# Optimization experiments

Measured on AMD Instinct MI355X. Metric: run time of the kernel, lower is better.

The kernel has to match this reference:

```python
import math
import jax, jax.numpy as jnp
import numpy as np

EMBED_DIM = 1024
NUM_HEADS = 16
HEAD_DIM = EMBED_DIM // NUM_HEADS


def _xavier(key, fan_in, fan_out):
    lim = math.sqrt(6.0 / (fan_in + fan_out))
    return jax.random.uniform(key, (fan_out, fan_in), jnp.float32, -lim, lim)


def setup_inputs() -> dict:
    key = jax.random.key(0)
    kx, kq, kk, kv, ko = jax.random.split(key, 5)
    B, L = 4, 2048
    x = jax.random.normal(kx, (B, L, EMBED_DIM), jnp.float32)
    return {
        "x": x,
        "wq": _xavier(kq, EMBED_DIM, EMBED_DIM), "bq": jnp.zeros((EMBED_DIM,), jnp.float32),
        "wk": _xavier(kk, EMBED_DIM, EMBED_DIM), "bk": jnp.zeros((EMBED_DIM,), jnp.float32),
        "wv": _xavier(kv, EMBED_DIM, EMBED_DIM), "bv": jnp.zeros((EMBED_DIM,), jnp.float32),
        "wo": _xavier(ko, EMBED_DIM, EMBED_DIM), "bo": jnp.zeros((EMBED_DIM,), jnp.float32),
    }


def reference(x, wq, bq, wk, bk, wv, bv, wo, bo):
    B, L, D = x.shape
    H, Dh = NUM_HEADS, HEAD_DIM

    def proj(w, b):
        # nn.Linear: x @ w.T + b, then split heads -> (B, H, L, Dh)
        return (jnp.einsum('bld,ed->ble', x, w) + b).reshape(B, L, H, Dh).transpose(0, 2, 1, 3)

    q, k, v = proj(wq, bq), proj(wk, bk), proj(wv, bv)
    # NOTE: original torch code scales by sqrt(key.size(dim=1)) == sqrt(num_heads)
    scale = 1.0 / math.sqrt(H)
    scores = jnp.einsum('bhqd,bhkd->bhqk', q, k) * scale  # (B, H, L, L)
    attn = jax.nn.softmax(scores, axis=-1)
    out = jnp.einsum('bhqk,bhkd->bhqd', attn, v)          # (B, H, L, Dh)
    out = out.transpose(0, 2, 1, 3).reshape(B, L, D)
    return jnp.einsum('bld,ed->ble', out, wo) + bo
```

## Files before the change

### kernel.cpp

```cpp
#include <hip/hip_runtime.h>
#include <hip/hip_bf16.h>

#define DEVI __device__ __forceinline__

using u16 = unsigned short;
typedef __attribute__((ext_vector_type(8))) short bf16x8;
typedef __attribute__((ext_vector_type(4))) short bf16x4;
typedef __attribute__((ext_vector_type(4))) float f32x4;

constexpr int Bb = 4, Ls = 2048, Dd = 1024, Hh = 16, DhC = 64;
constexpr int Mm = Bb * Ls;

DEVI u16 f2bf(float f) {
  union { float f; unsigned u; } x; x.f = f;
  unsigned r = x.u + 0x7FFFu + ((x.u >> 16) & 1u);
  return (u16)(r >> 16);
}
DEVI float bf2f(u16 b) {
  union { unsigned u; float f; } x; x.u = ((unsigned)b) << 16;
  return x.f;
}

DEVI unsigned cvt_pk_bf16(float a, float b) {
  unsigned d;
  asm("v_cvt_pk_bf16_f32 %0, %1, %2" : "=v"(d) : "v"(a), "v"(b));
  return d;
}

DEVI void gload_lds16(const u16* g, u16* l) {
  __builtin_amdgcn_global_load_lds(
      (const __attribute__((address_space(1))) unsigned int*)g,
      (__attribute__((address_space(3))) unsigned int*)l, 16, 0, 0);
}

DEVI bf16x8 ld_frag(const u16* p) { return *reinterpret_cast<const bf16x8*>(p); }

__global__ void cvt_all(const float* __restrict__ x,
                        const float* __restrict__ wq, const float* __restrict__ wk,
                        const float* __restrict__ wv, const float* __restrict__ wo,
                        u16* __restrict__ xb,
                        u16* __restrict__ wqb, u16* __restrict__ wkb,
                        u16* __restrict__ wvb, u16* __restrict__ wob) {
  const int tid = blockIdx.x * blockDim.x + threadIdx.x;
  constexpr int NT = 2048 * 256;
  constexpr int N4X = Mm * Dd / 4;
  constexpr int N4W = Dd * Dd / 4;
  for (int i = tid; i < N4X; i += NT) {
    float4 v = reinterpret_cast<const float4*>(x)[i];
    reinterpret_cast<ushort4*>(xb)[i] =
        make_ushort4(f2bf(v.x), f2bf(v.y), f2bf(v.z), f2bf(v.w));
  }
  for (int i = tid; i < 4 * N4W; i += NT) {
    int which = i / N4W, off = i - which * N4W;
    const float* s = which == 0 ? wq : which == 1 ? wk : which == 2 ? wv : wo;
    u16* d = which == 0 ? wqb : which == 1 ? wkb : which == 2 ? wvb : wob;
    float4 v = reinterpret_cast<const float4*>(s)[off];
    reinterpret_cast<ushort4*>(d)[off] =
        make_ushort4(f2bf(v.x), f2bf(v.y), f2bf(v.z), f2bf(v.w));
  }
}

__global__ __launch_bounds__(512) void gemm_qkv256(
    const u16* __restrict__ A, const u16* __restrict__ W,
    const float* __restrict__ bq, const float* __restrict__ bk2,
    const float* __restrict__ bv,
    u16* __restrict__ qm, u16* __restrict__ km, u16* __restrict__ vt)
{
  constexpr int K = 1024, BK = 64, NSTEP = K / BK;
  __shared__ u16 lds[2][2][256 * 64];

  const int tid = threadIdx.x;
  const int wave = tid >> 6, lane = tid & 63;
  const int wr = wave >> 2, wc = wave & 3;
  const int lrow = lane & 15, hi = lane >> 4, lk = hi * 8;
  const int swz = (lrow & 7) << 3;
  const int m0 = blockIdx.y * 256;
  const int n0g = blockIdx.x * 256;

  const int c_row[4] = { (0*512 + tid) >> 3, (1*512 + tid) >> 3,
                         (2*512 + tid) >> 3, (3*512 + tid) >> 3 };
  int c_kc[4];
#pragma unroll
  for (int p = 0; p < 4; ++p)
    c_kc[p] = (((p * 512 + tid) & 7) ^ (c_row[p] & 7)) * 8;

  f32x4 acc[8][4] = {};

#pragma unroll
  for (int p = 0; p < 4; ++p) {
    int c = p * 512 + tid;
    gload_lds16(A + (size_t)(m0 + c_row[p]) * K + c_kc[p], &lds[0][0][0] + c * 8);
    gload_lds16(W + (size_t)(n0g + c_row[p]) * K + c_kc[p], &lds[0][1][0] + c * 8);
  }
  __syncthreads();

  for (int t = 0; t < NSTEP; ++t) {
    const u16* Ab = &lds[t & 1][0][0];
    const u16* Bb = &lds[t & 1][1][0];
    u16* An = &lds[(t + 1) & 1][0][0];
    u16* Bn = &lds[(t + 1) & 1][1][0];
    const int k1 = (t + 1) * BK;
    const bool more = (t + 1 < NSTEP);

    bf16x8 a[4][2], b0[2][2], b1[2][2];

#define STAGE_Q(p)                                                             \
    if (more) {                                                                \
      int c = (p) * 512 + tid;                                                 \
      gload_lds16(A + (size_t)(m0 + c_row[p]) * K + k1 + c_kc[p], An + c * 8); \
      gload_lds16(W + (size_t)(n0g + c_row[p]) * K + k1 + c_kc[p], Bn + c * 8);\
    }

#pragma unroll
    for (int f = 0; f < 4; ++f) {
      int row = wr * 128 + f * 16 + lrow;
      a[f][0] = ld_frag(Ab + row * 64 + (lk ^ swz));
      a[f][1] = ld_frag(Ab + row * 64 + ((32 + lk) ^ swz));
    }
#pragma unroll
    for (int f = 0; f < 2; ++f) {
      int row = wc * 64 + f * 16 + lrow;
      b0[f][0] = ld_frag(Bb + row * 64 + (lk ^ swz));
      b0[f][1] = ld_frag(Bb + row * 64 + ((32 + lk) ^ swz));
    }
    STAGE_Q(0);
    __builtin_amdgcn_s_barrier();
    __builtin_amdgcn_s_setprio(1);
#pragma unroll
    for (int fm = 0; fm < 4; ++fm)
#pragma unroll
      for (int fn = 0; fn < 2; ++fn)
#pragma unroll
        for (int kk = 0; kk < 2; ++kk)
          acc[fm][fn] = __builtin_amdgcn_mfma_f32_16x16x32_bf16(a[fm][kk], b0[fn][kk], acc[fm][fn], 0, 0, 0);
    __builtin_amdgcn_s_setprio(0);
    __builtin_amdgcn_s_barrier();

#pragma unroll
    for (int f = 0; f < 2; ++f) {
      int row = wc * 64 + (2 + f) * 16 + lrow;
      b1[f][0] = ld_frag(Bb + row * 64 + (lk ^ swz));
      b1[f][1] = ld_frag(Bb + row * 64 + ((32 + lk) ^ swz));
    }
    STAGE_Q(1);
    __builtin_amdgcn_s_barrier();
    __builtin_amdgcn_s_setprio(1);
#pragma unroll
    for (int fm = 0; fm < 4; ++fm)
#pragma unroll
      for (int fn = 0; fn < 2; ++fn)
#pragma unroll
        for (int kk = 0; kk < 2; ++kk)
          acc[fm][2 + fn] = __builtin_amdgcn_mfma_f32_16x16x32_bf16(a[fm][kk], b1[fn][kk], acc[fm][2 + fn], 0, 0, 0);
    __builtin_amdgcn_s_setprio(0);
    __builtin_amdgcn_s_barrier();

#pragma unroll
    for (int f = 0; f < 4; ++f) {
      int row = wr * 128 + (4 + f) * 16 + lrow;
      a[f][0] = ld_frag(Ab + row * 64 + (lk ^ swz));
      a[f][1] = ld_frag(Ab + row * 64 + ((32 + lk) ^ swz));
    }
    STAGE_Q(2);
    __builtin_amdgcn_s_barrier();
    __builtin_amdgcn_s_setprio(1);
#pragma unroll
    for (int fm = 0; fm < 4; ++fm)
#pragma unroll
      for (int fn = 0; fn < 2; ++fn)
#pragma unroll
        for (int kk = 0; kk < 2; ++kk)
          acc[4 + fm][2 + fn] = __builtin_amdgcn_mfma_f32_16x16x32_bf16(a[fm][kk], b1[fn][kk], acc[4 + fm][2 + fn], 0, 0, 0);
    __builtin_amdgcn_s_setprio(0);
    __builtin_amdgcn_s_barrier();

    STAGE_Q(3);
    __builtin_amdgcn_s_barrier();
    __builtin_amdgcn_s_setprio(1);
#pragma unroll
    for (int fm = 0; fm < 4; ++fm)
#pragma unroll
      for (int fn = 0; fn < 2; ++fn)
#pragma unroll
        for (int kk = 0; kk < 2; ++kk)
          acc[4 + fm][fn] = __builtin_amdgcn_mfma_f32_16x16x32_bf16(a[fm][kk], b0[fn][kk], acc[4 + fm][fn], 0, 0, 0);
    __builtin_amdgcn_s_setprio(0);
    if (more) asm volatile("s_waitcnt vmcnt(0)" ::: "memory");
    __builtin_amdgcn_s_barrier();
#undef STAGE_Q
  }

  const int region = blockIdx.x >> 2;
  const int nc0 = (blockIdx.x & 3) * 256;
  const float* bias = region == 0 ? bq : region == 1 ? bk2 : bv;
  u16* dstRM = region == 0 ? qm : km;

#pragma unroll
  for (int fm = 0; fm < 8; ++fm) {
#pragma unroll
    for (int fn = 0; fn < 4; ++fn) {
      int row = m0 + wr * 128 + fm * 16 + hi * 4;
      int col = nc0 + wc * 64 + fn * 16 + lrow;
      float bv_ = bias[col];
      if (region == 2) {
        ushort4 o;
        o.x = f2bf(acc[fm][fn][0] + bv_); o.y = f2bf(acc[fm][fn][1] + bv_);
        o.z = f2bf(acc[fm][fn][2] + bv_); o.w = f2bf(acc[fm][fn][3] + bv_);
        *reinterpret_cast<ushort4*>(&vt[(size_t)col * Mm + row]) = o;
      } else {
#pragma unroll
        for (int j = 0; j < 4; ++j)
          dstRM[(size_t)(row + j) * Dd + col] = f2bf(acc[fm][fn][j] + bv_);
      }
    }
  }
}

__global__ __launch_bounds__(256) void gemm_out(
    const u16* __restrict__ A, const u16* __restrict__ Bt,
    const float* __restrict__ bias, float* __restrict__ C, int M, int N, int K)
{
  constexpr int BK = 64;
  __shared__ u16 As[128 * BK];
  __shared__ u16 Bs[128 * BK];
  const int tid = threadIdx.x;
  const int wave = tid >> 6, lane = tid & 63;
  const int wr = wave >> 1, wc = wave & 1;
  const int lrow = lane & 15, lk = (lane >> 4) * 8;
  const int m0 = blockIdx.y * 128, n0 = blockIdx.x * 128;
  const int srow = lane >> 3, scol = (lane & 7) * 8;

  f32x4 acc[4][4] = {};

  for (int k0 = 0; k0 < K; k0 += BK) {
    __syncthreads();
#pragma unroll
    for (int i = 0; i < 4; ++i) {
      int g = wave * 4 + i;
      int row = g * 8 + srow;
      gload_lds16(A  + (size_t)(m0 + row) * K + k0 + scol, As + g * 512);
      gload_lds16(Bt + (size_t)(n0 + row) * K + k0 + scol, Bs + g * 512);
    }
    __syncthreads();
#pragma unroll
    for (int kk = 0; kk < 2; ++kk) {
      bf16x8 af[4], bfr[4];
#pragma unroll
      for (int m = 0; m < 4; ++m) af[m]  = ld_frag(As + (wr*64 + m*16 + lrow)*BK + kk*32 + lk);
#pragma unroll
      for (int n = 0; n < 4; ++n) bfr[n] = ld_frag(Bs + (wc*64 + n*16 + lrow)*BK + kk*32 + lk);
      __builtin_amdgcn_s_setprio(1);
#pragma unroll
      for (int m = 0; m < 4; ++m)
#pragma unroll
        for (int n = 0; n < 4; ++n)
          acc[m][n] = __builtin_amdgcn_mfma_f32_16x16x32_bf16(af[m], bfr[n], acc[m][n], 0, 0, 0);
      __builtin_amdgcn_s_setprio(0);
    }
  }

#pragma unroll
  for (int m = 0; m < 4; ++m) {
#pragma unroll
    for (int n = 0; n < 4; ++n) {
      int row = m0 + wr*64 + m*16 + (lane >> 4) * 4;
      int col = n0 + wc*64 + n*16 + lrow;
      float bv = bias[col];
#pragma unroll
      for (int j = 0; j < 4; ++j)
        C[(size_t)(row + j) * N + col] = acc[m][n][j] + bv;
    }
  }
}

__global__ __launch_bounds__(512) void attn_fwd(
    const u16* __restrict__ Qm, const u16* __restrict__ Km,
    const u16* __restrict__ Vt, u16* __restrict__ Om)
{
  __shared__ u16 Ks[2][4096];
  __shared__ u16 Vs[2][4096];

  const int tid = threadIdx.x;
  const int wave = tid >> 6, lane = tid & 63;
  const int lrow = lane & 15, lk = (lane >> 4) * 8;
  const int swz = (lrow & 7) << 3;
  const int b = blockIdx.x >> 4, h = blockIdx.x & 15;
  const int rb = b * Ls;
  const int cb0 = h * DhC;
  const int q0 = blockIdx.y * 128;
  const int srow = lane >> 3;
  const int scol = ((lane & 7) ^ srow) * 8;

  const u16* kg = Km + (size_t)(rb + wave * 8 + srow) * Dd + cb0 + scol;
  const u16* vg = Vt + (size_t)(cb0 + wave * 8 + srow) * Mm + rb + scol;
  u16* ksflat = &Ks[0][0];
  u16* vsflat = &Vs[0][0];
  u16* ksl = ksflat + wave * 512;
  u16* vsl = vsflat + wave * 512;
  constexpr int LBUF = 4096;

#pragma unroll
  for (int g = 0; g < 2; ++g)
    gload_lds16(Qm + (size_t)(rb + q0 + wave * 16 + g * 8 + srow) * Dd + cb0 + scol,
                ksflat + (wave * 2 + g) * 512);
  gload_lds16(vg, vsl);
  __syncthreads();

  constexpr float SCL = 0.25f * 1.44269504088896f;
  bf16x8 aq0 = ld_frag(ksflat + (wave * 16 + lrow) * 64 + (lk ^ swz));
  bf16x8 aq1 = ld_frag(ksflat + (wave * 16 + lrow) * 64 + ((32 + lk) ^ swz));
#pragma unroll
  for (int e = 0; e < 8; e += 2) {
    unsigned d0 = cvt_pk_bf16(SCL * bf2f((u16)aq0[e]), SCL * bf2f((u16)aq0[e + 1]));
    unsigned d1 = cvt_pk_bf16(SCL * bf2f((u16)aq1[e]), SCL * bf2f((u16)aq1[e + 1]));
    aq0[e] = (short)(d0 & 0xffff); aq0[e + 1] = (short)(d0 >> 16);
    aq1[e] = (short)(d1 & 0xffff); aq1[e + 1] = (short)(d1 >> 16);
  }
  __syncthreads();
  gload_lds16(kg, ksl);
  __syncthreads();

  bf16x8 ones;
#pragma unroll
  for (int e = 0; e < 8; ++e) ones[e] = (short)0x3F80;

  f32x4 accO[4] = {};
  f32x4 acc_ps = {};

  int nb = 0;
  for (int kv0 = 0; kv0 < Ls; kv0 += 64) {
    if (kv0 + 64 < Ls) {
      int dst = (nb ^ 1) * LBUF;
      gload_lds16(kg + (size_t)(kv0 + 64) * Dd, ksl + dst);
      gload_lds16(vg + kv0 + 64, vsl + dst);
      asm volatile("s_waitcnt vmcnt(2)" ::: "memory");
    } else {
      asm volatile("s_waitcnt vmcnt(0)" ::: "memory");
    }
    __builtin_amdgcn_s_barrier();
    const u16* ks = ksflat + nb * LBUF;
    const u16* vs = vsflat + nb * LBUF;

    f32x4 s[4];
#pragma unroll
    for (int kb = 0; kb < 4; ++kb) {
      const u16* kr = ks + (kb * 16 + lrow) * 64;
      bf16x8 bk0 = ld_frag(kr + (lk ^ swz));
      bf16x8 bk1 = ld_frag(kr + ((32 + lk) ^ swz));
      f32x4 t = {};
      __builtin_amdgcn_s_setprio(1);
      t = __builtin_amdgcn_mfma_f32_16x16x32_bf16(bk0, aq0, t, 0, 0, 0);
      t = __builtin_amdgcn_mfma_f32_16x16x32_bf16(bk1, aq1, t, 0, 0, 0);
      __builtin_amdgcn_s_setprio(0);
      s[kb] = t;
    }

    unsigned u00 = cvt_pk_bf16(__builtin_amdgcn_exp2f(s[0][0]), __builtin_amdgcn_exp2f(s[0][1]));
    unsigned u01 = cvt_pk_bf16(__builtin_amdgcn_exp2f(s[0][2]), __builtin_amdgcn_exp2f(s[0][3]));
    unsigned u10 = cvt_pk_bf16(__builtin_amdgcn_exp2f(s[1][0]), __builtin_amdgcn_exp2f(s[1][1]));
    unsigned u11 = cvt_pk_bf16(__builtin_amdgcn_exp2f(s[1][2]), __builtin_amdgcn_exp2f(s[1][3]));
    unsigned u20 = cvt_pk_bf16(__builtin_amdgcn_exp2f(s[2][0]), __builtin_amdgcn_exp2f(s[2][1]));
    unsigned u21 = cvt_pk_bf16(__builtin_amdgcn_exp2f(s[2][2]), __builtin_amdgcn_exp2f(s[2][3]));
    unsigned u30 = cvt_pk_bf16(__builtin_amdgcn_exp2f(s[3][0]), __builtin_amdgcn_exp2f(s[3][1]));
    unsigned u31 = cvt_pk_bf16(__builtin_amdgcn_exp2f(s[3][2]), __builtin_amdgcn_exp2f(s[3][3]));

    asm("v_permlane32_swap_b32 %0, %1" : "+v"(u00), "+v"(u10));
    asm("v_permlane16_swap_b32 %0, %1" : "+v"(u00), "+v"(u10));
    asm("v_permlane32_swap_b32 %0, %1" : "+v"(u01), "+v"(u11));
    asm("v_permlane16_swap_b32 %0, %1" : "+v"(u01), "+v"(u11));
    asm("v_permlane32_swap_b32 %0, %1" : "+v"(u20), "+v"(u30));
    asm("v_permlane16_swap_b32 %0, %1" : "+v"(u20), "+v"(u30));
    asm("v_permlane32_swap_b32 %0, %1" : "+v"(u21), "+v"(u31));
    asm("v_permlane16_swap_b32 %0, %1" : "+v"(u21), "+v"(u31));

    union { unsigned u[4]; bf16x8 v; } apc0, apc1;
    apc0.u[0] = u00; apc0.u[1] = u01; apc0.u[2] = u10; apc0.u[3] = u11;
    apc1.u[0] = u20; apc1.u[1] = u21; apc1.u[2] = u30; apc1.u[3] = u31;

#pragma unroll
    for (int kk2 = 0; kk2 < 2; ++kk2) {
      bf16x8 ap = kk2 == 0 ? apc0.v : apc1.v;
      __builtin_amdgcn_s_setprio(1);
#pragma unroll
      for (int cb = 0; cb < 4; ++cb) {
        const u16* vr = vs + (cb * 16 + lrow) * 64;
        bf16x8 bv = ld_frag(vr + ((kk2 * 32 + lk) ^ swz));
        accO[cb] = __builtin_amdgcn_mfma_f32_16x16x32_bf16(bv, ap, accO[cb], 0, 0, 0);
      }
      acc_ps = __builtin_amdgcn_mfma_f32_16x16x32_bf16(ones, ap, acc_ps, 0, 0, 0);
      __builtin_amdgcn_s_setprio(0);
    }

    if (kv0 + 64 < Ls) __builtin_amdgcn_s_barrier();
    nb ^= 1;
  }

  float rinv = 1.0f / acc_ps[0];
  const size_t orow = (size_t)(rb + q0 + wave * 16 + lrow) * Dd + cb0;
#pragma unroll
  for (int cb = 0; cb < 4; ++cb) {
    uint2 o;
    o.x = cvt_pk_bf16(accO[cb][0] * rinv, accO[cb][1] * rinv);
    o.y = cvt_pk_bf16(accO[cb][2] * rinv, accO[cb][3] * rinv);
    *reinterpret_cast<uint2*>(&Om[orow + cb * 16 + (lk >> 1)]) = o;
  }
}

extern "C" void kernel_launch(void* const* d_in, const int* in_sizes, int n_in,
                              void* d_out, int out_size, void* d_ws, size_t ws_size,
                              hipStream_t stream) {
  (void)in_sizes; (void)n_in; (void)out_size; (void)ws_size;
  const float* x  = (const float*)d_in[0];
  const float* wq = (const float*)d_in[1];
  const float* bq = (const float*)d_in[2];
  const float* wk = (const float*)d_in[3];
  const float* bk = (const float*)d_in[4];
  const float* wv = (const float*)d_in[5];
  const float* bv = (const float*)d_in[6];
  const float* wo = (const float*)d_in[7];
  const float* bo = (const float*)d_in[8];
  float* out = (float*)d_out;

  u16* ws  = (u16*)d_ws;
  u16* xb  = ws;
  u16* wqb = xb  + (size_t)Mm * Dd;
  u16* wkb = wqb + (size_t)Dd * Dd;
  u16* wvb = wkb + (size_t)Dd * Dd;
  u16* wob = wvb + (size_t)Dd * Dd;
  u16* qm  = wob + (size_t)Dd * Dd;
  u16* km  = qm  + (size_t)Mm * Dd;
  u16* vt  = km  + (size_t)Mm * Dd;
  u16* om  = xb;

  cvt_all<<<2048, 256, 0, stream>>>(x, wq, wk, wv, wo, xb, wqb, wkb, wvb, wob);

  dim3 qkvgrid(3 * Dd / 256, Mm / 256);
  gemm_qkv256<<<qkvgrid, 512, 0, stream>>>(xb, wqb, bq, bk, bv, qm, km, vt);

  dim3 agrid(Bb * Hh, Ls / 128);
  attn_fwd<<<agrid, 512, 0, stream>>>(qm, km, vt, om);

  dim3 ogrid(Dd / 128, Mm / 128);
  gemm_out<<<ogrid, 256, 0, stream>>>(om, wob, bo, out, Mm, Dd, Dd);
}
```

Measured before the change: 197.2 us.

## Shrink QKV GEMM tile to 128x256 and add XCD-aware block remapping

Measured after the change: 194.0 us. About the same (-1.7%).

```diff
diff --git a/kernel.cpp b/kernel.cpp
--- a/kernel.cpp
+++ b/kernel.cpp
@@ -60,60 +60,65 @@
   }
 }
 
-__global__ __launch_bounds__(512) void gemm_qkv256(
+__global__ __launch_bounds__(512) void gemm_qkv(
     const u16* __restrict__ A, const u16* __restrict__ W,
     const float* __restrict__ bq, const float* __restrict__ bk2,
     const float* __restrict__ bv,
     u16* __restrict__ qm, u16* __restrict__ km, u16* __restrict__ vt)
 {
   constexpr int K = 1024, BK = 64, NSTEP = K / BK;
-  __shared__ u16 lds[2][2][256 * 64];
+  __shared__ u16 ldsA[2][128 * 64];
+  __shared__ u16 ldsB[2][256 * 64];
 
   const int tid = threadIdx.x;
   const int wave = tid >> 6, lane = tid & 63;
   const int wr = wave >> 2, wc = wave & 3;
   const int lrow = lane & 15, hi = lane >> 4, lk = hi * 8;
   const int swz = (lrow & 7) << 3;
-  const int m0 = blockIdx.y * 256;
-  const int n0g = blockIdx.x * 256;
-
-  const int c_row[4] = { (0*512 + tid) >> 3, (1*512 + tid) >> 3,
-                         (2*512 + tid) >> 3, (3*512 + tid) >> 3 };
-  int c_kc[4];
-#pragma unroll
-  for (int p = 0; p < 4; ++p)
-    c_kc[p] = (((p * 512 + tid) & 7) ^ (c_row[p] & 7)) * 8;
-
-  f32x4 acc[8][4] = {};
-
-#pragma unroll
-  for (int p = 0; p < 4; ++p) {
-    int c = p * 512 + tid;
-    gload_lds16(A + (size_t)(m0 + c_row[p]) * K + c_kc[p], &lds[0][0][0] + c * 8);
-    gload_lds16(W + (size_t)(n0g + c_row[p]) * K + c_kc[p], &lds[0][1][0] + c * 8);
-  }
+
+  const int lin = blockIdx.y * 12 + blockIdx.x;
+  const int nid = (lin & 7) * 96 + (lin >> 3);
+  const int bx = nid % 12, by = nid / 12;
+  const int m0 = by * 128;
+  const int n0g = bx * 256;
+
+  int a_row[2], a_kc[2], b_row[4], b_kc[4];
+#pragma unroll
+  for (int g = 0; g < 2; ++g) {
+    int c = g * 512 + tid;
+    a_row[g] = c >> 3;
+    a_kc[g] = ((c & 7) ^ (a_row[g] & 7)) * 8;
+  }
+#pragma unroll
+  for (int g = 0; g < 4; ++g) {
+    int c = g * 512 + tid;
+    b_row[g] = c >> 3;
+    b_kc[g] = ((c & 7) ^ (b_row[g] & 7)) * 8;
+  }
+
+  f32x4 acc[4][4] = {};
+
+#pragma unroll
+  for (int g = 0; g < 2; ++g)
+    gload_lds16(A + (size_t)(m0 + a_row[g]) * K + a_kc[g], &ldsA[0][0] + (g * 512 + tid) * 8);
+#pragma unroll
+  for (int g = 0; g < 4; ++g)
+    gload_lds16(W + (size_t)(n0g + b_row[g]) * K + b_kc[g], &ldsB[0][0] + (g * 512 + tid) * 8);
   __syncthreads();
 
   for (int t = 0; t < NSTEP; ++t) {
-    const u16* Ab = &lds[t & 1][0][0];
-    const u16* Bb = &lds[t & 1][1][0];
-    u16* An = &lds[(t + 1) & 1][0][0];
-    u16* Bn = &lds[(t + 1) & 1][1][0];
+    const u16* Ab = &ldsA[t & 1][0];
+    const u16* Bb = &ldsB[t & 1][0];
+    u16* An = &ldsA[(t + 1) & 1][0];
+    u16* Bn = &ldsB[(t + 1) & 1][0];
     const int k1 = (t + 1) * BK;
     const bool more = (t + 1 < NSTEP);
 
     bf16x8 a[4][2], b0[2][2], b1[2][2];
 
-#define STAGE_Q(p)                                                             \
-    if (more) {                                                                \
-      int c = (p) * 512 + tid;                                                 \
-      gload_lds16(A + (size_t)(m0 + c_row[p]) * K + k1 + c_kc[p], An + c * 8); \
-      gload_lds16(W + (size_t)(n0g + c_row[p]) * K + k1 + c_kc[p], Bn + c * 8);\
-    }
-
 #pragma unroll
     for (int f = 0; f < 4; ++f) {
-      int row = wr * 128 + f * 16 + lrow;
+      int row = wr * 64 + f * 16 + lrow;
       a[f][0] = ld_frag(Ab + row * 64 + (lk ^ swz));
       a[f][1] = ld_frag(Ab + row * 64 + ((32 + lk) ^ swz));
     }
@@ -123,7 +128,11 @@
       b0[f][0] = ld_frag(Bb + row * 64 + (lk ^ swz));
       b0[f][1] = ld_frag(Bb + row * 64 + ((32 + lk) ^ swz));
     }
-    STAGE_Q(0);
+    if (more) {
+      gload_lds16(A + (size_t)(m0 + a_row[0]) * K + k1 + a_kc[0], An + (0 * 512 + tid) * 8);
+      gload_lds16(A + (size_t)(m0 + a_row[1]) * K + k1 + a_kc[1], An + (1 * 512 + tid) * 8);
+      gload_lds16(W + (size_t)(n0g + b_row[0]) * K + k1 + b_kc[0], Bn + (0 * 512 + tid) * 8);
+    }
     __builtin_amdgcn_s_barrier();
     __builtin_amdgcn_s_setprio(1);
 #pragma unroll
@@ -142,7 +151,11 @@
       b1[f][0] = ld_frag(Bb + row * 64 + (lk ^ swz));
       b1[f][1] = ld_frag(Bb + row * 64 + ((32 + lk) ^ swz));
     }
-    STAGE_Q(1);
+    if (more) {
+      gload_lds16(W + (size_t)(n0g + b_row[1]) * K + k1 + b_kc[1], Bn + (1 * 512 + tid) * 8);
+      gload_lds16(W + (size_t)(n0g + b_row[2]) * K + k1 + b_kc[2], Bn + (2 * 512 + tid) * 8);
+      gload_lds16(W + (size_t)(n0g + b_row[3]) * K + k1 + b_kc[3], Bn + (3 * 512 + tid) * 8);
+    }
     __builtin_amdgcn_s_barrier();
     __builtin_amdgcn_s_setprio(1);
 #pragma unroll
@@ -153,53 +166,20 @@
         for (int kk = 0; kk < 2; ++kk)
           acc[fm][2 + fn] = __builtin_amdgcn_mfma_f32_16x16x32_bf16(a[fm][kk], b1[fn][kk], acc[fm][2 + fn], 0, 0, 0);
     __builtin_amdgcn_s_setprio(0);
-    __builtin_amdgcn_s_barrier();
-
-#pragma unroll
-    for (int f = 0; f < 4; ++f) {
-      int row = wr * 128 + (4 + f) * 16 + lrow;
-      a[f][0] = ld_frag(Ab + row * 64 + (lk ^ swz));
-      a[f][1] = ld_frag(Ab + row * 64 + ((32 + lk) ^ swz));
-    }
-    STAGE_Q(2);
-    __builtin_amdgcn_s_barrier();
-    __builtin_amdgcn_s_setprio(1);
-#pragma unroll
-    for (int fm = 0; fm < 4; ++fm)
-#pragma unroll
-      for (int fn = 0; fn < 2; ++fn)
-#pragma unroll
-        for (int kk = 0; kk < 2; ++kk)
-          acc[4 + fm][2 + fn] = __builtin_amdgcn_mfma_f32_16x16x32_bf16(a[fm][kk], b1[fn][kk], acc[4 + fm][2 + fn], 0, 0, 0);
-    __builtin_amdgcn_s_setprio(0);
-    __builtin_amdgcn_s_barrier();
-
-    STAGE_Q(3);
-    __builtin_amdgcn_s_barrier();
-    __builtin_amdgcn_s_setprio(1);
-#pragma unroll
-    for (int fm = 0; fm < 4; ++fm)
-#pragma unroll
-      for (int fn = 0; fn < 2; ++fn)
-#pragma unroll
-        for (int kk = 0; kk < 2; ++kk)
-          acc[4 + fm][fn] = __builtin_amdgcn_mfma_f32_16x16x32_bf16(a[fm][kk], b0[fn][kk], acc[4 + fm][fn], 0, 0, 0);
-    __builtin_amdgcn_s_setprio(0);
     if (more) asm volatile("s_waitcnt vmcnt(0)" ::: "memory");
     __builtin_amdgcn_s_barrier();
-#undef STAGE_Q
-  }
-
-  const int region = blockIdx.x >> 2;
-  const int nc0 = (blockIdx.x & 3) * 256;
+  }
+
+  const int region = bx >> 2;
+  const int nc0 = (bx & 3) * 256;
   const float* bias = region == 0 ? bq : region == 1 ? bk2 : bv;
   u16* dstRM = region == 0 ? qm : km;
 
 #pragma unroll
-  for (int fm = 0; fm < 8; ++fm) {
+  for (int fm = 0; fm < 4; ++fm) {
 #pragma unroll
     for (int fn = 0; fn < 4; ++fn) {
-      int row = m0 + wr * 128 + fm * 16 + hi * 4;
+      int row = m0 + wr * 64 + fm * 16 + hi * 4;
       int col = nc0 + wc * 64 + fn * 16 + lrow;
       float bv_ = bias[col];
       if (region == 2) {
@@ -434,8 +414,8 @@
 
   cvt_all<<<2048, 256, 0, stream>>>(x, wq, wk, wv, wo, xb, wqb, wkb, wvb, wob);
 
-  dim3 qkvgrid(3 * Dd / 256, Mm / 256);
-  gemm_qkv256<<<qkvgrid, 512, 0, stream>>>(xb, wqb, bq, bk, bv, qm, km, vt);
+  dim3 qkvgrid(3 * Dd / 256, Mm / 128);
+  gemm_qkv<<<qkvgrid, 512, 0, stream>>>(xb, wqb, bq, bk, bv, qm, km, vt);
 
   dim3 agrid(Bb * Hh, Ls / 128);
   attn_fwd<<<agrid, 512, 0, stream>>>(qm, km, vt, om);
```
